# Optimization experiments

Measured on AMD Instinct MI355X. Metric: run time of the kernel, lower is better.

## Reference

```python
import jax, jax.numpy as jnp
import numpy as np

B, N, D = 2, 8192, 64          # batch, points, feature dim (dim_in == dim_out)
FILTER_SIZE = 11               # k nearest neighbors in feature space
N_ITER = 5                     # mean-field iterations


def setup_inputs() -> dict:
    key = jax.random.key(0)
    k0, k1, k2, k3 = jax.random.split(key, 4)
    return {
        "logits": jax.random.normal(k0, (B, N), jnp.float32),
        "p": jax.random.normal(k1, (B, D, N), jnp.float32),
        "W1": jax.random.normal(k2, (D, D), jnp.float32) / np.float32(np.sqrt(D)),
        "b1": jnp.zeros((D,), jnp.float32),
        "W2": jax.random.normal(k3, (D, D), jnp.float32) / np.float32(np.sqrt(D)),
        "b2": jnp.zeros((D,), jnp.float32),
    }


def reference(logits, p, W1, b1, W2, b2):
    # crf_encoder: two stacked Linear layers applied to p.permute(0,2,1) -> [B,N,D]
    f = jnp.einsum('bdn,de->bne', p, W1) + b1
    f = jnp.einsum('bne,ef->bnf', f, W2) + b2  # [B,N,D] feature embedding

    # pairwise squared distances in feature space: [B,N,N]
    sq = jnp.sum(f * f, axis=-1)
    d2 = sq[:, :, None] + sq[:, None, :] - 2.0 * jnp.einsum('bnd,bmd->bnm', f, f)

    # filter_size nearest neighbors (includes self) with Gaussian weights exp(-d2)
    neg_d2, idx = jax.lax.top_k(-d2, FILTER_SIZE)   # [B,N,K]
    w = jnp.exp(neg_d2)                             # [B,N,K]

    gather = jax.vmap(lambda qb, ib: qb[ib])        # per-batch gather: [N],[N,K]->[N,K]

    # mean-field iterations (binary CRF: sigmoid marginals, unary = logits)
    u = logits
    for _ in range(N_ITER):
        q = jax.nn.sigmoid(u)                       # current marginals [B,N]
        msg = jnp.sum(w * gather(q, idx), axis=-1)  # filtered message   [B,N]
        u = logits - msg                            # compatibility transform + unary

    return jax.nn.sigmoid(u)  # return_log_proba=False -> probabilities, [B,N]
```

## Files before the change

### kernel.cpp

```cpp
#include <hip/hip_runtime.h>

#define NPTS 8192
#define NTOT 16384
#define KNB 11
#define CAP 16
#define MARG 9.0f
#define QMAX 2048
#define NTILE 1056

typedef __attribute__((ext_vector_type(8))) short short8;
typedef __attribute__((ext_vector_type(4))) float f32x4;

__device__ __forceinline__ unsigned short f2bf(float x) {
  union { float f; unsigned u; } v; v.f = x;
  unsigned r = v.u + 0x7FFFu + ((v.u >> 16) & 1u);
  return (unsigned short)(r >> 16);
}

__device__ __forceinline__ float sigm(float x) { return 1.f / (1.f + expf(-x)); }

__device__ __forceinline__ void st_cg(unsigned* p, unsigned v) {
  __hip_atomic_store(p, v, __ATOMIC_RELAXED, __HIP_MEMORY_SCOPE_AGENT);
}
__device__ __forceinline__ void st_cg(int* p, int v) {
  __hip_atomic_store(p, v, __ATOMIC_RELAXED, __HIP_MEMORY_SCOPE_AGENT);
}
__device__ __forceinline__ unsigned ld_cg(const unsigned* p) {
  return __hip_atomic_load(p, __ATOMIC_RELAXED, __HIP_MEMORY_SCOPE_AGENT);
}
__device__ __forceinline__ int ld_cg(const int* p) {
  return __hip_atomic_load(p, __ATOMIC_RELAXED, __HIP_MEMORY_SCOPE_AGENT);
}

__global__ __launch_bounds__(256) void k1_encode(
    const float* __restrict__ p,
    const float* __restrict__ W1,
    const float* __restrict__ b1,
    const float* __restrict__ W2,
    const float* __restrict__ b2,
    const float* __restrict__ logits,
    float* __restrict__ out,
    float* __restrict__ f32f,
    unsigned short* __restrict__ fpre,
    float* __restrict__ sq,
    float* __restrict__ sq32,
    unsigned* __restrict__ cnt,
    int* __restrict__ lctr,
    unsigned* __restrict__ done) {
  __shared__ float sp[64 * 64];
  __shared__ float st[64 * 65];
  __shared__ float sPart[4][64];
  int t = threadIdx.x, lane = t & 63;
  int w = __builtin_amdgcn_readfirstlane(t >> 6);
  int e0 = w * 16;
  int base = blockIdx.x * 64;
  int b = base >> 13, n0 = base & (NPTS - 1);
  const float* pb = p + (size_t)b * 64 * NPTS + n0;

  if (w == 0) {
    cnt[base + lane] = 0u;
    float lg = logits[base + lane];
    float u = lg;
#pragma unroll
    for (int it = 0; it < 5; ++it) u = lg - sigm(u);
    out[base + lane] = sigm(u);
  }
  if (blockIdx.x == 0) {
    done[t] = 0u;
    if (t == 0) *lctr = 0;
  }

  int row = t >> 4, chunk = t & 15;
#pragma unroll
  for (int k = 0; k < 4; ++k) {
    int r = k * 16 + row;
    uint4 v = *(const uint4*)(pb + (size_t)r * NPTS + chunk * 4);
    *(uint4*)(sp + r * 64 + chunk * 4) = v;
  }
  __syncthreads();

  float tt[16];
#pragma unroll
  for (int j = 0; j < 16; ++j) tt[j] = b1[e0 + j];
#pragma unroll 8
  for (int d = 0; d < 64; ++d) {
    float pd = sp[d * 64 + lane];
#pragma unroll
    for (int j = 0; j < 16; ++j)
      tt[j] = fmaf(pd, W1[d * 64 + e0 + j], tt[j]);
  }
#pragma unroll
  for (int j = 0; j < 16; ++j) st[lane * 65 + e0 + j] = tt[j];
  __syncthreads();

  float f[16];
#pragma unroll
  for (int j = 0; j < 16; ++j) f[j] = b2[e0 + j];
#pragma unroll 8
  for (int d = 0; d < 64; ++d) {
    float td = st[lane * 65 + d];
#pragma unroll
    for (int j = 0; j < 16; ++j)
      f[j] = fmaf(td, W2[d * 64 + e0 + j], f[j]);
  }

  float s = 0.f;
#pragma unroll
  for (int j = 0; j < 16; ++j) s = fmaf(f[j], f[j], s);
  sPart[w][lane] = s;
  __syncthreads();
  if (w == 0) {
    float s32 = sPart[0][lane] + sPart[1][lane];
    float s64 = s32 + (sPart[2][lane] + sPart[3][lane]);
    sq32[base + lane] = s32;
    sq[base + lane] = s64;
  }

  f32x4* o4 = (f32x4*)(f32f + (size_t)(base + lane) * 64 + e0);
#pragma unroll
  for (int jj = 0; jj < 4; ++jj) {
    f32x4 v; v[0] = f[4 * jj]; v[1] = f[4 * jj + 1]; v[2] = f[4 * jj + 2]; v[3] = f[4 * jj + 3];
    o4[jj] = v;
  }
  if (w < 2) {
    unsigned* ob = (unsigned*)(fpre + (size_t)(base + lane) * 32 + e0);
#pragma unroll
    for (int jj = 0; jj < 8; ++jj) {
      unsigned lo = f2bf(f[2 * jj]);
      unsigned hi = f2bf(f[2 * jj + 1]);
      ob[jj] = lo | (hi << 16);
    }
  }
}

union SMK {
  uint4 sB[1024];
  struct { float qs[QMAX]; float su[QMAX]; int sl[QMAX]; } c;
};

__global__ __launch_bounds__(256) void k2e(
    const unsigned short* __restrict__ fpre,
    const float* __restrict__ sq32,
    unsigned* __restrict__ cnt,
    unsigned* __restrict__ cand,
    int* __restrict__ lctr,
    int* __restrict__ list,
    unsigned* __restrict__ done,
    const float* __restrict__ f32f, const float* __restrict__ sq,
    int* __restrict__ rowmap,
    float* __restrict__ Wbuf,
    int* __restrict__ IDXs,
    const float* __restrict__ logits, float* __restrict__ out) {
  __shared__ SMK sm;
  __shared__ int slast;
  int t = threadIdx.x;
  int bid = blockIdx.x;

  {
    int b = (bid >= 528) ? 1 : 0;
    int rem = bid - b * 528;
    int band = (int)((sqrtf(8.f * (float)rem + 1.f) - 1.f) * 0.5f);
    if (((band + 1) * (band + 2)) / 2 <= rem) band++;
    else if ((band * (band + 1)) / 2 > rem) band--;
    int seg = rem - (band * (band + 1)) / 2;

    int lane = t & 63;
    int arow = lane & 15;
    int q = lane >> 4;
    int wave = t >> 6;
    int rowbase = band * 256 + wave * 64;
    int cbase = seg * 256;
    const unsigned short* fb = fpre + (size_t)b * NPTS * 32;
    const float* s32b = sq32 + b * NPTS;

    const uint4* gsrc = (const uint4*)fb + (size_t)seg * 1024;
    uint4 v[4];
#pragma unroll
    for (int k = 0; k < 4; ++k) v[k] = gsrc[t + k * 256];

    short8 afrag[4];
#pragma unroll
    for (int tr = 0; tr < 4; ++tr)
      afrag[tr] = *(const short8*)(fb + (size_t)(rowbase + tr * 16 + arow) * 32 + q * 8);

    f32x4 srq[4], nh[4];
#pragma unroll
    for (int tr = 0; tr < 4; ++tr) {
      srq[tr] = *(const f32x4*)(s32b + rowbase + tr * 16 + (q << 2));
      nh[tr] = -0.5f * srq[tr];
    }
    float thrc[16];
#pragma unroll
    for (int cc = 0; cc < 4; ++cc)
#pragma unroll
      for (int tc = 0; tc < 4; ++tc)
        thrc[cc * 4 + tc] = 0.5f * s32b[cbase + cc * 64 + tc * 16 + arow] - 0.5f * MARG;

#pragma unroll
    for (int k = 0; k < 4; ++k) {
      int c = t + k * 256;
      int r = c >> 2, qq = c & 3;
      sm.sB[r * 4 + (qq ^ (r & 3))] = v[k];
    }
    __syncthreads();

    unsigned hitmask = 0u;
#pragma unroll
    for (int cc = 0; cc < 4; ++cc)
#pragma unroll
      for (int tc = 0; tc < 4; ++tc) {
        int e = cc * 4 + tc;
        int rl = cc * 64 + tc * 16 + arow;
        short8 bf = *(const short8*)&sm.sB[rl * 4 + (q ^ (rl & 3))];
        f32x4 a0 = __builtin_amdgcn_mfma_f32_16x16x32_bf16(afrag[0], bf, nh[0], 0, 0, 0);
        f32x4 a1 = __builtin_amdgcn_mfma_f32_16x16x32_bf16(afrag[1], bf, nh[1], 0, 0, 0);
        f32x4 a2 = __builtin_amdgcn_mfma_f32_16x16x32_bf16(afrag[2], bf, nh[2], 0, 0, 0);
        f32x4 a3 = __builtin_amdgcn_mfma_f32_16x16x32_bf16(afrag[3], bf, nh[3], 0, 0, 0);
        float m0 = fmaxf(fmaxf(a0[0], a0[1]), fmaxf(a0[2], a0[3]));
        float m1 = fmaxf(fmaxf(a1[0], a1[1]), fmaxf(a1[2], a1[3]));
        float m2 = fmaxf(fmaxf(a2[0], a2[1]), fmaxf(a2[2], a2[3]));
        float m3 = fmaxf(fmaxf(a3[0], a3[1]), fmaxf(a3[2], a3[3]));
        float m = fmaxf(fmaxf(m0, m1), fmaxf(m2, m3));
        if (__ballot(m > thrc[e])) hitmask |= (1u << e);
      }

    if (hitmask) {
#pragma unroll 1
      for (int e = 0; e < 16; ++e) {
        if (!(hitmask & (1u << e))) continue;
        int cc = e >> 2, tc = e & 3;
        int rl = cc * 64 + tc * 16 + arow;
        short8 bf = *(const short8*)&sm.sB[rl * 4 + (q ^ (rl & 3))];
        int colpt = cbase + cc * 64 + tc * 16 + arow;
        float scv = s32b[colpt];
        f32x4 acc[4];
#pragma unroll
        for (int tr = 0; tr < 4; ++tr)
          acc[tr] = __builtin_amdgcn_mfma_f32_16x16x32_bf16(afrag[tr], bf, nh[tr], 0, 0, 0);
#pragma unroll
        for (int tr = 0; tr < 4; ++tr)
#pragma unroll
          for (int rg = 0; rg < 4; ++rg) {
            float d2 = scv - 2.f * acc[tr][rg];
            if (d2 < MARG) {
              int rowpt = rowbase + tr * 16 + (q << 2) + rg;
              int gr = b * NPTS + rowpt;
              union { float f; unsigned u; } cv; cv.f = d2 + 16.f;
              unsigned kb = cv.u & 0xFFFFE000u;
              unsigned slot = atomicAdd(&cnt[gr], 1u);
              if (slot < CAP) st_cg(&cand[gr * CAP + slot], kb | (unsigned)colpt);
              if (slot == 1u) {
                int ls = atomicAdd(lctr, 1);
                if (ls < QMAX * 4) st_cg(&list[ls], gr);
              }
              if (band != seg) {
                int gc = b * NPTS + colpt;
                unsigned slot2 = atomicAdd(&cnt[gc], 1u);
                if (slot2 < CAP) st_cg(&cand[gc * CAP + slot2], kb | (unsigned)rowpt);
                if (slot2 == 1u) {
                  int ls2 = atomicAdd(lctr, 1);
                  if (ls2 < QMAX * 4) st_cg(&list[ls2], gc);
                }
              }
            }
          }
      }
    }
  }

  __syncthreads();
  if (t == 0) {
    int last = 0;
    asm volatile("s_waitcnt vmcnt(0)" ::: "memory");
    unsigned o = atomicAdd(&done[(bid & 7) * 32], 1u);
    if (o == 131u) {
      unsigned o2 = atomicAdd(&done[8], 1u);
      if (o2 == 7u) last = 1;
    }
    slast = last;
  }
  __syncthreads();
  if (!slast) return;

  int nm = ld_cg(lctr); if (nm > QMAX) nm = QMAX;

#pragma unroll 1
  for (int k = t; k < nm; k += 256) {
    int r = ld_cg(&list[k]);
    sm.c.sl[k] = r;
    rowmap[r] = k;
    sm.c.qs[k] = sigm(logits[r]);
  }
  __syncthreads();

#pragma unroll 1
  for (int k = t; k < nm; k += 256) {
    int r = sm.c.sl[k];
    int b = r >> 13;
    unsigned count = ld_cg(&cnt[r]);
    if (count > CAP) count = CAP;

    unsigned kc[CAP];
#pragma unroll
    for (int j = 0; j < CAP; ++j)
      kc[j] = (j < (int)count) ? ld_cg(&cand[r * CAP + j]) : 0xFFFFFFFFu;
#pragma unroll
    for (int a = 0; a < CAP - 1; ++a)
#pragma unroll
      for (int c = 0; c < CAP - 1; ++c) {
        unsigned lo = min(kc[c], kc[c + 1]);
        unsigned hi = max(kc[c], kc[c + 1]);
        kc[c] = lo; kc[c + 1] = hi;
      }

    float fr[64];
    const f32x4* fr4 = (const f32x4*)(f32f + (size_t)r * 64);
#pragma unroll
    for (int j = 0; j < 16; ++j) {
      f32x4 v = fr4[j];
      fr[4 * j] = v[0]; fr[4 * j + 1] = v[1]; fr[4 * j + 2] = v[2]; fr[4 * j + 3] = v[3];
    }
    float sqr = sq[r];
    int nsel = (int)count < KNB ? (int)count : KNB;
#pragma unroll
    for (int kk = 0; kk < KNB; ++kk) {
      float wgt = 0.f;
      int gi = r;
      if (kk < nsel) {
        int col = (int)(kc[kk] & 8191u);
        gi = b * NPTS + col;
        const float* fm = f32f + (size_t)gi * 64;
        float dot = 0.f;
#pragma unroll
        for (int d = 0; d < 64; ++d) dot = fmaf(fr[d], fm[d], dot);
        float d2 = sqr + sq[gi] - 2.f * dot;
        wgt = expf(-d2);
      }
      Wbuf[k * KNB + kk] = wgt;
      IDXs[k * KNB + kk] = rowmap[gi] & (QMAX - 1);
    }
  }
  __syncthreads();

  for (int it = 0; it < 5; ++it) {
#pragma unroll 1
    for (int k = t; k < nm; k += 256) {
      float msg = 0.f;
      const float* wp = Wbuf + k * KNB;
      const int* ip = IDXs + k * KNB;
#pragma unroll
      for (int kk = 0; kk < KNB; ++kk) msg = fmaf(wp[kk], sm.c.qs[ip[kk]], msg);
      sm.c.su[k] = logits[sm.c.sl[k]] - msg;
    }
    __syncthreads();
#pragma unroll 1
    for (int k = t; k < nm; k += 256) sm.c.qs[k] = sigm(sm.c.su[k]);
    __syncthreads();
  }
#pragma unroll 1
  for (int k = t; k < nm; k += 256) out[sm.c.sl[k]] = sigm(sm.c.su[k]);
}

extern "C" void kernel_launch(void* const* d_in, const int* in_sizes, int n_in,
                              void* d_out, int out_size, void* d_ws, size_t ws_size,
                              hipStream_t stream) {
  const float* logits = (const float*)d_in[0];
  const float* p      = (const float*)d_in[1];
  const float* W1     = (const float*)d_in[2];
  const float* b1     = (const float*)d_in[3];
  const float* W2     = (const float*)d_in[4];
  const float* b2     = (const float*)d_in[5];
  float* out = (float*)d_out;

  char* ws = (char*)d_ws;
  float* f32f = (float*)ws;
  unsigned short* fpre = (unsigned short*)(f32f + (size_t)NTOT * 64);
  float* sq = (float*)(fpre + (size_t)NTOT * 32);
  float* sq32 = sq + NTOT;
  unsigned* cnt = (unsigned*)(sq32 + NTOT);
  unsigned* cand = cnt + NTOT;
  int* lctr = (int*)(cand + (size_t)NTOT * CAP);
  unsigned* done = (unsigned*)(lctr + 1);
  int* list = (int*)(done + 256);
  int* rowmap = list + QMAX * 4;
  float* Wbuf = (float*)(rowmap + NTOT);
  int* IDXs = (int*)(Wbuf + (size_t)QMAX * KNB);

  k1_encode<<<256, 256, 0, stream>>>(p, W1, b1, W2, b2, logits, out,
                                     f32f, fpre, sq, sq32, cnt, lctr, done);
  k2e<<<NTILE, 256, 0, stream>>>(fpre, sq32, cnt, cand, lctr, list, done,
                                 f32f, sq, rowmap, Wbuf, IDXs, logits, out);
}
```

Baseline: 110.9 us.

## Fuse encoder and distance kernels into one launch with ticket-ordered dataflow flags

Merges the encoder kernel into the distance/CRF kernel. Blocks take an atomic ticket, so the first 256 tickets compute feature tiles and publish per-tile ready flags. Each distance tile spins until its row and column feature tiles are flagged, which lets encoding overlap with distance work and removes a kernel launch boundary. Counters and flags move to device globals that the last block resets at the end of the call. This adds spin-wait and cross-block ordering risk, plus reliance on the in-kernel reset for the next call.

```diff
diff --git a/kernel.cpp b/kernel.cpp
--- a/kernel.cpp
+++ b/kernel.cpp
@@ -11,6 +11,12 @@
 typedef __attribute__((ext_vector_type(8))) short short8;
 typedef __attribute__((ext_vector_type(4))) float f32x4;
 
+__device__ unsigned g_ticket;
+__device__ int g_flags[256];
+__device__ unsigned g_done[260];
+__device__ int g_lctr;
+__device__ unsigned g_cnt[NTOT];
+
 __device__ __forceinline__ unsigned short f2bf(float x) {
   union { float f; unsigned u; } v; v.f = x;
   unsigned r = v.u + 0x7FFFu + ((v.u >> 16) & 1u);
@@ -19,151 +25,159 @@
 
 __device__ __forceinline__ float sigm(float x) { return 1.f / (1.f + expf(-x)); }
 
-__device__ __forceinline__ void st_cg(unsigned* p, unsigned v) {
+__device__ __forceinline__ void st_cg4u(unsigned* p, unsigned v) {
   __hip_atomic_store(p, v, __ATOMIC_RELAXED, __HIP_MEMORY_SCOPE_AGENT);
 }
-__device__ __forceinline__ void st_cg(int* p, int v) {
+__device__ __forceinline__ void st_cg4f(float* p, float v) {
+  union { float f; unsigned u; } c; c.f = v;
+  __hip_atomic_store((unsigned*)p, c.u, __ATOMIC_RELAXED, __HIP_MEMORY_SCOPE_AGENT);
+}
+__device__ __forceinline__ void st_cg8(unsigned long long* p, unsigned long long v) {
   __hip_atomic_store(p, v, __ATOMIC_RELAXED, __HIP_MEMORY_SCOPE_AGENT);
 }
-__device__ __forceinline__ unsigned ld_cg(const unsigned* p) {
+__device__ __forceinline__ unsigned ld_cg4u(const unsigned* p) {
   return __hip_atomic_load(p, __ATOMIC_RELAXED, __HIP_MEMORY_SCOPE_AGENT);
 }
-__device__ __forceinline__ int ld_cg(const int* p) {
+__device__ __forceinline__ int ld_cg4i(const int* p) {
   return __hip_atomic_load(p, __ATOMIC_RELAXED, __HIP_MEMORY_SCOPE_AGENT);
 }
 
-__global__ __launch_bounds__(256) void k1_encode(
-    const float* __restrict__ p,
-    const float* __restrict__ W1,
-    const float* __restrict__ b1,
-    const float* __restrict__ W2,
-    const float* __restrict__ b2,
-    const float* __restrict__ logits,
-    float* __restrict__ out,
-    float* __restrict__ f32f,
-    unsigned short* __restrict__ fpre,
-    float* __restrict__ sq,
-    float* __restrict__ sq32,
-    unsigned* __restrict__ cnt,
-    int* __restrict__ lctr,
-    unsigned* __restrict__ done) {
-  __shared__ float sp[64 * 64];
-  __shared__ float st[64 * 65];
-  __shared__ float sPart[4][64];
-  int t = threadIdx.x, lane = t & 63;
-  int w = __builtin_amdgcn_readfirstlane(t >> 6);
-  int e0 = w * 16;
-  int base = blockIdx.x * 64;
-  int b = base >> 13, n0 = base & (NPTS - 1);
-  const float* pb = p + (size_t)b * 64 * NPTS + n0;
-
-  if (w == 0) {
-    cnt[base + lane] = 0u;
-    float lg = logits[base + lane];
-    float u = lg;
-#pragma unroll
-    for (int it = 0; it < 5; ++it) u = lg - sigm(u);
-    out[base + lane] = sigm(u);
-  }
-  if (blockIdx.x == 0) {
-    done[t] = 0u;
-    if (t == 0) *lctr = 0;
-  }
-
-  int row = t >> 4, chunk = t & 15;
-#pragma unroll
-  for (int k = 0; k < 4; ++k) {
-    int r = k * 16 + row;
-    uint4 v = *(const uint4*)(pb + (size_t)r * NPTS + chunk * 4);
-    *(uint4*)(sp + r * 64 + chunk * 4) = v;
-  }
-  __syncthreads();
-
-  float tt[16];
-#pragma unroll
-  for (int j = 0; j < 16; ++j) tt[j] = b1[e0 + j];
-#pragma unroll 8
-  for (int d = 0; d < 64; ++d) {
-    float pd = sp[d * 64 + lane];
-#pragma unroll
-    for (int j = 0; j < 16; ++j)
-      tt[j] = fmaf(pd, W1[d * 64 + e0 + j], tt[j]);
-  }
-#pragma unroll
-  for (int j = 0; j < 16; ++j) st[lane * 65 + e0 + j] = tt[j];
-  __syncthreads();
-
-  float f[16];
-#pragma unroll
-  for (int j = 0; j < 16; ++j) f[j] = b2[e0 + j];
-#pragma unroll 8
-  for (int d = 0; d < 64; ++d) {
-    float td = st[lane * 65 + d];
-#pragma unroll
-    for (int j = 0; j < 16; ++j)
-      f[j] = fmaf(td, W2[d * 64 + e0 + j], f[j]);
-  }
-
-  float s = 0.f;
-#pragma unroll
-  for (int j = 0; j < 16; ++j) s = fmaf(f[j], f[j], s);
-  sPart[w][lane] = s;
-  __syncthreads();
-  if (w == 0) {
-    float s32 = sPart[0][lane] + sPart[1][lane];
-    float s64 = s32 + (sPart[2][lane] + sPart[3][lane]);
-    sq32[base + lane] = s32;
-    sq[base + lane] = s64;
-  }
-
-  f32x4* o4 = (f32x4*)(f32f + (size_t)(base + lane) * 64 + e0);
-#pragma unroll
-  for (int jj = 0; jj < 4; ++jj) {
-    f32x4 v; v[0] = f[4 * jj]; v[1] = f[4 * jj + 1]; v[2] = f[4 * jj + 2]; v[3] = f[4 * jj + 3];
-    o4[jj] = v;
-  }
-  if (w < 2) {
-    unsigned* ob = (unsigned*)(fpre + (size_t)(base + lane) * 32 + e0);
-#pragma unroll
-    for (int jj = 0; jj < 8; ++jj) {
-      unsigned lo = f2bf(f[2 * jj]);
-      unsigned hi = f2bf(f[2 * jj + 1]);
-      ob[jj] = lo | (hi << 16);
-    }
-  }
-}
-
-union SMK {
+union SMF {
+  struct { float sp[64 * 64]; float st[64 * 65]; float sPart[4][64]; } a;
   uint4 sB[1024];
   struct { float qs[QMAX]; float su[QMAX]; int sl[QMAX]; } c;
 };
 
-__global__ __launch_bounds__(256) void k2e(
-    const unsigned short* __restrict__ fpre,
-    const float* __restrict__ sq32,
-    unsigned* __restrict__ cnt,
-    unsigned* __restrict__ cand,
-    int* __restrict__ lctr,
-    int* __restrict__ list,
-    unsigned* __restrict__ done,
-    const float* __restrict__ f32f, const float* __restrict__ sq,
-    int* __restrict__ rowmap,
-    float* __restrict__ Wbuf,
-    int* __restrict__ IDXs,
-    const float* __restrict__ logits, float* __restrict__ out) {
-  __shared__ SMK sm;
+__global__ __launch_bounds__(256) void fuse(
+    const float* __restrict__ p, const float* __restrict__ W1,
+    const float* __restrict__ b1, const float* __restrict__ W2,
+    const float* __restrict__ b2, const float* __restrict__ logits,
+    float* __restrict__ out,
+    float* __restrict__ f32f, unsigned short* __restrict__ fpre,
+    float* __restrict__ sq, float* __restrict__ sq32,
+    unsigned* __restrict__ cand, int* __restrict__ list,
+    int* __restrict__ rowmap, float* __restrict__ Wbuf, int* __restrict__ IDXs) {
+  __shared__ SMF sm;
+  __shared__ int stk;
   __shared__ int slast;
   int t = threadIdx.x;
   int bid = blockIdx.x;
 
+  if (t == 0) stk = (int)atomicAdd(&g_ticket, 1u);
+  __syncthreads();
+  int tk = stk;
+
+  if (tk < 256) {
+    int lane = t & 63;
+    int w = __builtin_amdgcn_readfirstlane(t >> 6);
+    int e0 = w * 16;
+    int base = tk * 64;
+    int b = base >> 13, n0 = base & (NPTS - 1);
+    const float* pb = p + (size_t)b * 64 * NPTS + n0;
+
+    int row = t >> 4, chunk = t & 15;
+#pragma unroll
+    for (int k = 0; k < 4; ++k) {
+      int r = k * 16 + row;
+      uint4 v = *(const uint4*)(pb + (size_t)r * NPTS + chunk * 4);
+      *(uint4*)(sm.a.sp + r * 64 + chunk * 4) = v;
+    }
+    __syncthreads();
+
+    float tt[16];
+#pragma unroll
+    for (int j = 0; j < 16; ++j) tt[j] = b1[e0 + j];
+#pragma unroll 8
+    for (int d = 0; d < 64; ++d) {
+      float pd = sm.a.sp[d * 64 + lane];
+#pragma unroll
+      for (int j = 0; j < 16; ++j)
+        tt[j] = fmaf(pd, W1[d * 64 + e0 + j], tt[j]);
+    }
+#pragma unroll
+    for (int j = 0; j < 16; ++j) sm.a.st[lane * 65 + e0 + j] = tt[j];
+    __syncthreads();
+
+    float f[16];
+#pragma unroll
+    for (int j = 0; j < 16; ++j) f[j] = b2[e0 + j];
+#pragma unroll 8
+    for (int d = 0; d < 64; ++d) {
+      float td = sm.a.st[lane * 65 + d];
+#pragma unroll
+      for (int j = 0; j < 16; ++j)
+        f[j] = fmaf(td, W2[d * 64 + e0 + j], f[j]);
+    }
+
+    float s = 0.f;
+#pragma unroll
+    for (int j = 0; j < 16; ++j) s = fmaf(f[j], f[j], s);
+    sm.a.sPart[w][lane] = s;
+    __syncthreads();
+    if (w == 0) {
+      float s32 = sm.a.sPart[0][lane] + sm.a.sPart[1][lane];
+      float s64 = s32 + (sm.a.sPart[2][lane] + sm.a.sPart[3][lane]);
+      st_cg4f(&sq32[base + lane], s32);
+      st_cg4f(&sq[base + lane], s64);
+      float lg = logits[base + lane];
+      float u = lg;
+#pragma unroll
+      for (int it = 0; it < 5; ++it) u = lg - sigm(u);
+      st_cg4f(&out[base + lane], sigm(u));
+    }
+
+    unsigned long long* o8 =
+        (unsigned long long*)(f32f + (size_t)(base + lane) * 64 + e0);
+#pragma unroll
+    for (int jj = 0; jj < 8; ++jj) {
+      union { float f; unsigned u; } lo, hi;
+      lo.f = f[2 * jj]; hi.f = f[2 * jj + 1];
+      st_cg8(&o8[jj], (unsigned long long)lo.u |
+                      ((unsigned long long)hi.u << 32));
+    }
+    if (w < 2) {
+      unsigned long long* ob =
+          (unsigned long long*)(fpre + (size_t)(base + lane) * 32 + e0);
+#pragma unroll
+      for (int jj = 0; jj < 4; ++jj) {
+        unsigned w0 = (unsigned)f2bf(f[4 * jj]) |
+                      ((unsigned)f2bf(f[4 * jj + 1]) << 16);
+        unsigned w1 = (unsigned)f2bf(f[4 * jj + 2]) |
+                      ((unsigned)f2bf(f[4 * jj + 3]) << 16);
+        st_cg8(&ob[jj], (unsigned long long)w0 |
+                        ((unsigned long long)w1 << 32));
+      }
+    }
+    asm volatile("s_waitcnt vmcnt(0)" ::: "memory");
+    __syncthreads();
+    if (t == 0)
+      __hip_atomic_store(&g_flags[tk], 1, __ATOMIC_RELAXED,
+                         __HIP_MEMORY_SCOPE_AGENT);
+  }
+
+  int b = (bid >= 528) ? 1 : 0;
+  int rem = bid - b * 528;
+  int band = (int)((sqrtf(8.f * (float)rem + 1.f) - 1.f) * 0.5f);
+  if (((band + 1) * (band + 2)) / 2 <= rem) band++;
+  else if ((band * (band + 1)) / 2 > rem) band--;
+  int seg = rem - (band * (band + 1)) / 2;
+
   {
-    int b = (bid >= 528) ? 1 : 0;
-    int rem = bid - b * 528;
-    int band = (int)((sqrtf(8.f * (float)rem + 1.f) - 1.f) * 0.5f);
-    if (((band + 1) * (band + 2)) / 2 <= rem) band++;
-    else if ((band * (band + 1)) / 2 > rem) band--;
-    int seg = rem - (band * (band + 1)) / 2;
-
+    int c0 = b * 128 + band * 4, c1 = b * 128 + seg * 4;
+    if (t == 0) {
+      for (long it2 = 0; it2 < 100000000L; ++it2) {
+        int ok = ld_cg4i(&g_flags[c0]) & ld_cg4i(&g_flags[c0 + 1]) &
+                 ld_cg4i(&g_flags[c0 + 2]) & ld_cg4i(&g_flags[c0 + 3]) &
+                 ld_cg4i(&g_flags[c1]) & ld_cg4i(&g_flags[c1 + 1]) &
+                 ld_cg4i(&g_flags[c1 + 2]) & ld_cg4i(&g_flags[c1 + 3]);
+        if (ok) break;
+        __builtin_amdgcn_s_sleep(1);
+      }
+    }
+    __syncthreads();
+  }
+
+  {
     int lane = t & 63;
     int arow = lane & 15;
     int q = lane >> 4;
@@ -196,6 +210,7 @@
       for (int tc = 0; tc < 4; ++tc)
         thrc[cc * 4 + tc] = 0.5f * s32b[cbase + cc * 64 + tc * 16 + arow] - 0.5f * MARG;
 
+    __syncthreads();
 #pragma unroll
     for (int k = 0; k < 4; ++k) {
       int c = t + k * 256;
@@ -247,19 +262,21 @@
               int gr = b * NPTS + rowpt;
               union { float f; unsigned u; } cv; cv.f = d2 + 16.f;
               unsigned kb = cv.u & 0xFFFFE000u;
-              unsigned slot = atomicAdd(&cnt[gr], 1u);
-              if (slot < CAP) st_cg(&cand[gr * CAP + slot], kb | (unsigned)colpt);
+              unsigned slot = atomicAdd(&g_cnt[gr], 1u);
+              if (slot < CAP) st_cg4u(&cand[gr * CAP + slot], kb | (unsigned)colpt);
               if (slot == 1u) {
-                int ls = atomicAdd(lctr, 1);
-                if (ls < QMAX * 4) st_cg(&list[ls], gr);
+                int ls = atomicAdd(&g_lctr, 1);
+                if (ls < QMAX * 4) __hip_atomic_store(&list[ls], gr, __ATOMIC_RELAXED,
+                                                      __HIP_MEMORY_SCOPE_AGENT);
               }
               if (band != seg) {
                 int gc = b * NPTS + colpt;
-                unsigned slot2 = atomicAdd(&cnt[gc], 1u);
-                if (slot2 < CAP) st_cg(&cand[gc * CAP + slot2], kb | (unsigned)rowpt);
+                unsigned slot2 = atomicAdd(&g_cnt[gc], 1u);
+                if (slot2 < CAP) st_cg4u(&cand[gc * CAP + slot2], kb | (unsigned)rowpt);
                 if (slot2 == 1u) {
-                  int ls2 = atomicAdd(lctr, 1);
-                  if (ls2 < QMAX * 4) st_cg(&list[ls2], gc);
+                  int ls2 = atomicAdd(&g_lctr, 1);
+                  if (ls2 < QMAX * 4) __hip_atomic_store(&list[ls2], gc, __ATOMIC_RELAXED,
+                                                         __HIP_MEMORY_SCOPE_AGENT);
                 }
               }
             }
@@ -268,13 +285,13 @@
     }
   }
 
+  asm volatile("s_waitcnt vmcnt(0)" ::: "memory");
   __syncthreads();
   if (t == 0) {
     int last = 0;
-    asm volatile("s_waitcnt vmcnt(0)" ::: "memory");
-    unsigned o = atomicAdd(&done[(bid & 7) * 32], 1u);
+    unsigned o = atomicAdd(&g_done[(bid & 7) * 32], 1u);
     if (o == 131u) {
-      unsigned o2 = atomicAdd(&done[8], 1u);
+      unsigned o2 = atomicAdd(&g_done[256], 1u);
       if (o2 == 7u) last = 1;
     }
     slast = last;
@@ -282,11 +299,11 @@
   __syncthreads();
   if (!slast) return;
 
-  int nm = ld_cg(lctr); if (nm > QMAX) nm = QMAX;
+  int nm = ld_cg4i(&g_lctr); if (nm > QMAX) nm = QMAX;
 
 #pragma unroll 1
   for (int k = t; k < nm; k += 256) {
-    int r = ld_cg(&list[k]);
+    int r = ld_cg4i(&list[k]);
     sm.c.sl[k] = r;
     rowmap[r] = k;
     sm.c.qs[k] = sigm(logits[r]);
@@ -296,14 +313,14 @@
 #pragma unroll 1
   for (int k = t; k < nm; k += 256) {
     int r = sm.c.sl[k];
-    int b = r >> 13;
-    unsigned count = ld_cg(&cnt[r]);
+    int bb = r >> 13;
+    unsigned count = ld_cg4u(&g_cnt[r]);
     if (count > CAP) count = CAP;
 
     unsigned kc[CAP];
 #pragma unroll
     for (int j = 0; j < CAP; ++j)
-      kc[j] = (j < (int)count) ? ld_cg(&cand[r * CAP + j]) : 0xFFFFFFFFu;
+      kc[j] = (j < (int)count) ? ld_cg4u(&cand[r * CAP + j]) : 0xFFFFFFFFu;
 #pragma unroll
     for (int a = 0; a < CAP - 1; ++a)
 #pragma unroll
@@ -328,7 +345,7 @@
       int gi = r;
       if (kk < nsel) {
         int col = (int)(kc[kk] & 8191u);
-        gi = b * NPTS + col;
+        gi = bb * NPTS + col;
         const float* fm = f32f + (size_t)gi * 64;
         float dot = 0.f;
 #pragma unroll
@@ -358,7 +375,14 @@
     __syncthreads();
   }
 #pragma unroll 1
-  for (int k = t; k < nm; k += 256) out[sm.c.sl[k]] = sigm(sm.c.su[k]);
+  for (int k = t; k < nm; k += 256) st_cg4f(&out[sm.c.sl[k]], sigm(sm.c.su[k]));
+
+#pragma unroll 1
+  for (int k = t; k < NTOT; k += 256) g_cnt[k] = 0u;
+#pragma unroll 1
+  for (int k = t; k < 260; k += 256) g_done[k] = 0u;
+  if (t < 256) g_flags[t] = 0;
+  if (t == 0) { g_lctr = 0; g_ticket = 0u; }
 }
 
 extern "C" void kernel_launch(void* const* d_in, const int* in_sizes, int n_in,
@@ -377,17 +401,13 @@
   unsigned short* fpre = (unsigned short*)(f32f + (size_t)NTOT * 64);
   float* sq = (float*)(fpre + (size_t)NTOT * 32);
   float* sq32 = sq + NTOT;
-  unsigned* cnt = (unsigned*)(sq32 + NTOT);
-  unsigned* cand = cnt + NTOT;
-  int* lctr = (int*)(cand + (size_t)NTOT * CAP);
-  unsigned* done = (unsigned*)(lctr + 1);
-  int* list = (int*)(done + 256);
+  unsigned* cand = (unsigned*)(sq32 + NTOT);
+  int* list = (int*)(cand + (size_t)NTOT * CAP);
   int* rowmap = list + QMAX * 4;
   float* Wbuf = (float*)(rowmap + NTOT);
   int* IDXs = (int*)(Wbuf + (size_t)QMAX * KNB);
 
-  k1_encode<<<256, 256, 0, stream>>>(p, W1, b1, W2, b2, logits, out,
-                                     f32f, fpre, sq, sq32, cnt, lctr, done);
-  k2e<<<NTILE, 256, 0, stream>>>(fpre, sq32, cnt, cand, lctr, list, done,
-                                 f32f, sq, rowmap, Wbuf, IDXs, logits, out);
-}
+  fuse<<<NTILE, 256, 0, stream>>>(p, W1, b1, W2, b2, logits, out,
+                                  f32f, fpre, sq, sq32, cand, list,
+                                  rowmap, Wbuf, IDXs);
+}
```

New measurement: 128.4 us. 1.16x slower.
